# Kernel tuning notes

Measured on AMD Instinct MI355X. Metric: run time of the kernel, lower is better.

Reference implementation:

```python
import jax, jax.numpy as jnp
import numpy as np

EMBED = 1024
HEADS = 16
HDIM = EMBED // HEADS  # k_dim == v_dim == 64
MAXPOS = 256
L = 2 * MAXPOS  # rpe table length = 512
B, S = 1, 2048
EPS = 1e-6


def setup_inputs() -> dict:
    key = jax.random.key(0)
    ks = jax.random.split(key, 16)
    def xavier(k, shape):
        fan_in, fan_out = shape[1], shape[0]
        std = (2.0 / (fan_in + fan_out)) ** 0.5
        return jax.random.normal(k, shape, dtype=jnp.float32) * std
    inp = {
        "query": jax.random.normal(ks[0], (B, S, EMBED), dtype=jnp.float32),
        "key":   jax.random.normal(ks[1], (B, S, EMBED), dtype=jnp.float32),
        "value": jax.random.normal(ks[2], (B, S, EMBED), dtype=jnp.float32),
        "pos":   jax.random.randint(ks[3], (B, S, S), 0, L, dtype=jnp.int32),
        "mask":  jnp.ones((B, S, S), dtype=jnp.float32),
        # projections (stored as [out, in] like torch Linear)
        "Wq": xavier(ks[4], (HEADS * HDIM, EMBED)), "bq": jnp.zeros((HEADS * HDIM,), jnp.float32),
        "Wk": xavier(ks[5], (HEADS * HDIM, EMBED)), "bk": jnp.zeros((HEADS * HDIM,), jnp.float32),
        "Wv": xavier(ks[6], (HEADS * HDIM, EMBED)), "bv": jnp.zeros((HEADS * HDIM,), jnp.float32),
        "rpe": jnp.zeros((L, HEADS, HDIM), jnp.float32) + 0.02 * jax.random.normal(ks[7], (L, HEADS, HDIM), dtype=jnp.float32),
        "Wqt": xavier(ks[8], (EMBED, EMBED)), "bqt": jnp.zeros((EMBED,), jnp.float32),
        "Wo": xavier(ks[9], (EMBED, HEADS * HDIM)), "bo": jnp.zeros((EMBED,), jnp.float32),
        "gamma": jnp.ones((EMBED,), jnp.float32),
        "beta": jnp.zeros((EMBED,), jnp.float32),
    }
    return inp


def _layer_norm(x, gamma, beta):
    mu = jnp.mean(x, axis=-1, keepdims=True)
    var = jnp.mean(jnp.square(x - mu), axis=-1, keepdims=True)
    return (x - mu) * jax.lax.rsqrt(var + EPS) * gamma + beta


def reference(query, key, value, pos, mask, Wq, bq, Wk, bk, Wv, bv, rpe, Wqt, bqt, Wo, bo, gamma, beta):
    b, s, _ = query.shape
    scaling = HDIM ** (-0.5)
    q = (query @ Wq.T + bq) * scaling          # [b,s,n*d]
    k = key @ Wk.T + bk
    v = value @ Wv.T + bv
    q = q.reshape(b, s, HEADS, HDIM)
    k = k.reshape(b, s, HEADS, HDIM)
    v = v.reshape(b, s, HEADS, HDIM)
    attn = jnp.einsum('bqnd,bknd->bqkn', q, k)          # [b,q,k,n]
    qrpe = jnp.einsum('bqnd,lnd->bqln', q, rpe)         # [b,q,L,n]
    idx = jnp.broadcast_to(pos[..., None], (b, s, s, HEADS))
    qrpe_g = jnp.take_along_axis(qrpe, idx, axis=2)     # gather per (q,k) pair
    attn = attn + qrpe_g
    attn = attn - (1.0 - mask[..., None]) * 1e6
    attn = jax.nn.softmax(attn, axis=-2)                # softmax over key axis
    out = jnp.einsum('bqkn,bknd->bqnd', attn, v).reshape(b, s, HEADS * HDIM)
    out = (out @ Wo.T + bo) + (query @ Wqt.T + bqt)
    return _layer_norm(out, gamma, beta)
```

## Files before the change

### kernel.cpp

```cpp
#include <hip/hip_runtime.h>


typedef short          bf16x8 __attribute__((ext_vector_type(8)));
typedef float          f32x4  __attribute__((ext_vector_type(4)));
typedef int            i32x4  __attribute__((ext_vector_type(4)));
typedef unsigned short u16x4  __attribute__((ext_vector_type(4)));
typedef unsigned short u16x8  __attribute__((ext_vector_type(8)));
typedef unsigned int   u32x2  __attribute__((ext_vector_type(2)));

#define SEQ 2048
#define EMB 1024
#define NH  16
#define HD  64
#define RL  512

#define MFMA16(a,b,c) __builtin_amdgcn_mfma_f32_16x16x32_bf16((a),(b),(c),0,0,0)

__device__ __forceinline__ unsigned short f2bf(float f){
  union{float f; unsigned u;} x; x.f=f;
  unsigned r = x.u + 0x7FFFu + ((x.u>>16)&1u);
  return (unsigned short)(r>>16);
}
__device__ __forceinline__ unsigned cvtpk(float a, float b){
  unsigned r;
  asm("v_cvt_pk_bf16_f32 %0, %1, %2" : "=v"(r) : "v"(a), "v"(b));
  return r;
}
__device__ __forceinline__ float fexp2(float x){
  float r; asm("v_exp_f32 %0, %1" : "=v"(r) : "v"(x)); return r;
}
__device__ __forceinline__ unsigned char f2e5(float f){
  union{_Float16 h; unsigned short u;} cv; cv.h = (_Float16)f;
  unsigned short b = cv.u;
  unsigned r = (unsigned)b + 0x7Fu + ((b>>8)&1u);
  return (unsigned char)(r>>8);
}
__device__ __forceinline__ float e52f(unsigned short b){
  union{unsigned short u; _Float16 h;} cv; cv.u = (unsigned short)(b<<8);
  return (float)cv.h;
}
__device__ __forceinline__ void gload16(const void* g, void* l){
  __builtin_amdgcn_global_load_lds((const __attribute__((address_space(1))) unsigned int*)g,
                                   (__attribute__((address_space(3))) unsigned int*)l, 16, 0, 0);
}
__device__ __forceinline__ bf16x8 fragld(const unsigned short* t, int row, int chunk){
  int swz = chunk ^ (row & 7);
  return *(const bf16x8*)(t + row*64 + swz*8);
}

__global__ __launch_bounds__(256) void cvt_all(
    const float* __restrict__ s0, const float* __restrict__ s1, const float* __restrict__ s2,
    const float* __restrict__ s3, const float* __restrict__ s4, const float* __restrict__ s5,
    const float* __restrict__ s6, const float* __restrict__ s7,
    unsigned short* __restrict__ d0, unsigned short* __restrict__ d1, unsigned short* __restrict__ d2,
    unsigned short* __restrict__ d3, unsigned short* __restrict__ d4, unsigned short* __restrict__ d5,
    unsigned short* __restrict__ d6, unsigned short* __restrict__ d7,
    const float* __restrict__ rpe, unsigned short* __restrict__ rpe_bf)
{
  if (blockIdx.y == 8) {
    int i = (blockIdx.x*256 + threadIdx.x)*4;
    if (i >= RL*NH*HD) return;
    int l = i >> 10, h = (i >> 6) & 15, d = i & 63;
    f32x4 a = *(const f32x4*)(rpe + i);
    u16x4 o;
    #pragma unroll
    for (int j=0;j<4;++j) o[j]=f2bf(a[j]);
    *(u16x4*)(rpe_bf + ((size_t)h*RL + l)*HD + d) = o;
    return;
  }
  const float* s; unsigned short* d; int n;
  switch (blockIdx.y) {
    case 0: s=s0; d=d0; n=SEQ*EMB; break;
    case 1: s=s1; d=d1; n=SEQ*EMB; break;
    case 2: s=s2; d=d2; n=SEQ*EMB; break;
    case 3: s=s3; d=d3; n=EMB*EMB; break;
    case 4: s=s4; d=d4; n=EMB*EMB; break;
    case 5: s=s5; d=d5; n=EMB*EMB; break;
    case 6: s=s6; d=d6; n=EMB*EMB; break;
    default: s=s7; d=d7; n=EMB*EMB; break;
  }
  int i = (blockIdx.x*256 + threadIdx.x)*8;
  if (i >= n) return;
  f32x4 a = *(const f32x4*)(s+i);
  f32x4 b = *(const f32x4*)(s+i+4);
  u16x8 o;
  #pragma unroll
  for (int j=0;j<4;++j){ o[j]=f2bf(a[j]); o[4+j]=f2bf(b[j]); }
  *(u16x8*)(d+i) = o;
}

__global__ __launch_bounds__(256) void pack_pm(const int* __restrict__ pos,
                                               const float* __restrict__ mask,
                                               unsigned short* __restrict__ pm)
{
  int i = (blockIdx.x*256 + threadIdx.x)*8;
  i32x4 p0 = *(const i32x4*)(pos + i);
  i32x4 p1 = *(const i32x4*)(pos + i + 4);
  f32x4 m0 = *(const f32x4*)(mask + i);
  f32x4 m1 = *(const f32x4*)(mask + i + 4);
  u16x4 lo, hi;
  #pragma unroll
  for (int j=0;j<4;++j){
    lo[j] = (m0[j] > 0.5f) ? (unsigned short)p0[j] : (unsigned short)512;
    hi[j] = (m1[j] > 0.5f) ? (unsigned short)p1[j] : (unsigned short)512;
  }
  int grp = i & ~31;
  int o0  = ((i & 15) >> 2)*8 + ((i >> 4) & 1)*4;
  *(u16x4*)(pm + grp + o0)     = lo;
  *(u16x4*)(pm + grp + o0 + 8) = hi;
}

__device__ __forceinline__ void gemm_core(const unsigned short* __restrict__ A,
                                          const unsigned short* __restrict__ W,
                                          unsigned short* At, unsigned short* Wt,
                                          f32x4 acc[4][4], int m0, int n0)
{
  const int tid = threadIdx.x, lane = tid & 63, w = tid >> 6;
  const int rg = lane >> 3, sc = (lane & 7) ^ rg;
  const int c = lane & 15, g = lane >> 4;
  const int wm = w >> 1, wn = w & 1;

  for (int kt = 0; kt < EMB/64; ++kt) {
    __syncthreads();
    #pragma unroll
    for (int i = 0; i < 4; ++i) {
      int r = w*32 + i*8 + rg;
      gload16(A + (size_t)(m0+r)*EMB + kt*64 + sc*8, At + (w*32 + i*8)*64);
      gload16(W + (size_t)(n0+r)*EMB + kt*64 + sc*8, Wt + (w*32 + i*8)*64);
    }
    __syncthreads();
    #pragma unroll
    for (int kk = 0; kk < 2; ++kk) {
      bf16x8 af[4], bw[4];
      #pragma unroll
      for (int mf = 0; mf < 4; ++mf) af[mf] = fragld(At, wm*64 + mf*16 + c, kk*4 + g);
      #pragma unroll
      for (int nf = 0; nf < 4; ++nf) bw[nf] = fragld(Wt, wn*64 + nf*16 + c, kk*4 + g);
      __builtin_amdgcn_s_setprio(1);
      #pragma unroll
      for (int mf = 0; mf < 4; ++mf)
        #pragma unroll
        for (int nf = 0; nf < 4; ++nf)
          acc[mf][nf] = MFMA16(af[mf], bw[nf], acc[mf][nf]);
      __builtin_amdgcn_s_setprio(0);
    }
  }
}

__global__ __launch_bounds__(256) void gemm_proj(
    const unsigned short* __restrict__ Aq, const unsigned short* __restrict__ Ak,
    const unsigned short* __restrict__ Av,
    const unsigned short* __restrict__ Wq, const unsigned short* __restrict__ Wk,
    const unsigned short* __restrict__ Wv, const unsigned short* __restrict__ Wqt,
    const float* __restrict__ bq, const float* __restrict__ bk,
    const float* __restrict__ bv, const float* __restrict__ bqt,
    unsigned short* __restrict__ q_out, unsigned short* __restrict__ k_out,
    unsigned short* __restrict__ vt_out, float* __restrict__ qt_out)
{
  __shared__ alignas(16) unsigned short At[128*64];
  __shared__ alignas(16) unsigned short Wt[128*64];
  const unsigned short *A, *W; const float* bias;
  const int z = blockIdx.z;
  if      (z == 0) { A=Aq; W=Wq;  bias=bq;  }
  else if (z == 1) { A=Ak; W=Wk;  bias=bk;  }
  else if (z == 2) { A=Av; W=Wv;  bias=bv;  }
  else             { A=Aq; W=Wqt; bias=bqt; }

  f32x4 acc[4][4];
  #pragma unroll
  for (int i=0;i<4;++i)
    #pragma unroll
    for (int j=0;j<4;++j) acc[i][j] = (f32x4){0.f,0.f,0.f,0.f};

  const int m0 = blockIdx.y*128, n0 = blockIdx.x*128;
  gemm_core(A, W, At, Wt, acc, m0, n0);

  const int lane = threadIdx.x & 63, w = threadIdx.x >> 6;
  const int c = lane & 15, g = lane >> 4, wm = w >> 1, wn = w & 1;
  const float QSCALE = 0.125f * 1.4426950408889634f;
  #pragma unroll
  for (int nf = 0; nf < 4; ++nf) {
    int n = n0 + wn*64 + nf*16 + c;
    float b = bias[n];
    #pragma unroll
    for (int mf = 0; mf < 4; ++mf) {
      int mb = m0 + wm*64 + mf*16 + g*4;
      if (z == 0) {
        #pragma unroll
        for (int j=0;j<4;++j) q_out[(size_t)(mb+j)*EMB + n] = f2bf((acc[mf][nf][j] + b)*QSCALE);
      } else if (z == 1) {
        #pragma unroll
        for (int j=0;j<4;++j) k_out[(size_t)(mb+j)*EMB + n] = f2bf(acc[mf][nf][j] + b);
      } else if (z == 2) {
        u16x4 pk;
        #pragma unroll
        for (int j=0;j<4;++j) pk[j] = f2bf(acc[mf][nf][j] + b);
        *(u16x4*)(vt_out + (size_t)n*SEQ + mb) = pk;
      } else {
        #pragma unroll
        for (int j=0;j<4;++j) qt_out[(size_t)(mb+j)*EMB + n] = acc[mf][nf][j] + b;
      }
    }
  }
}

__global__ __launch_bounds__(256) void gemm_wo(
    const unsigned short* __restrict__ A, const unsigned short* __restrict__ W,
    const float* __restrict__ bo, float* __restrict__ qt)
{
  __shared__ alignas(16) unsigned short At[128*64];
  __shared__ alignas(16) unsigned short Wt[128*64];
  f32x4 acc[4][4];
  #pragma unroll
  for (int i=0;i<4;++i)
    #pragma unroll
    for (int j=0;j<4;++j) acc[i][j] = (f32x4){0.f,0.f,0.f,0.f};
  const int m0 = blockIdx.y*128, n0 = blockIdx.x*128;
  gemm_core(A, W, At, Wt, acc, m0, n0);

  const int lane = threadIdx.x & 63, w = threadIdx.x >> 6;
  const int c = lane & 15, g = lane >> 4, wm = w >> 1, wn = w & 1;
  #pragma unroll
  for (int nf = 0; nf < 4; ++nf) {
    int n = n0 + wn*64 + nf*16 + c;
    float b = bo[n];
    #pragma unroll
    for (int mf = 0; mf < 4; ++mf) {
      int mb = m0 + wm*64 + mf*16 + g*4;
      #pragma unroll
      for (int j=0;j<4;++j) {
        size_t idx = (size_t)(mb+j)*EMB + n;
        qt[idx] = acc[mf][nf][j] + b + qt[idx];
      }
    }
  }
}

__global__ __launch_bounds__(256) void attn_kernel(
    const unsigned short* __restrict__ q_bf, const unsigned short* __restrict__ k_bf,
    const unsigned short* __restrict__ vt_bf, const unsigned short* __restrict__ rpe_bf,
    const unsigned short* __restrict__ pm, unsigned short* __restrict__ att_out)
{
  __shared__ alignas(16) unsigned char pool[38144];
  unsigned short* k_tile  = (unsigned short*)(pool);
  unsigned short* vt_tile = (unsigned short*)(pool + 8192);
  unsigned char*  table8  = pool + 16384;
  unsigned short* q_tile  = (unsigned short*)(pool + 33024);
  unsigned short* p_base  = (unsigned short*)(pool + 33024);
  float*          red     = (float*)(pool);
  float*          red2    = (float*)(pool + 8192);

  const int tid = threadIdx.x, lane = tid & 63, w = tid >> 6;
  const int qh = w & 1, ks = w >> 1;
  const int h = blockIdx.y;
  const int q0 = blockIdx.x * 32;
  const int rg = lane >> 3, sc = (lane & 7) ^ rg;
  const int c = lane & 15, g = lane >> 4;
  const bf16x8 kOnes = {16256,16256,16256,16256,16256,16256,16256,16256};

  gload16(q_bf + (size_t)(q0 + w*8 + rg)*EMB + h*HD + sc*8, q_tile + (w*8)*64);
  __syncthreads();

  for (int ch = 0; ch < 8; ++ch) {
    __syncthreads();
    #pragma unroll
    for (int i = 0; i < 2; ++i)
      gload16(rpe_bf + ((size_t)h*RL + ch*64 + w*16 + i*8 + rg)*HD + sc*8,
              k_tile + (w*16 + i*8)*64);
    __syncthreads();
    #pragma unroll
    for (int qq = 0; qq < 2; ++qq) {
      f32x4 dd = (f32x4){0.f,0.f,0.f,0.f};
      dd = MFMA16(fragld(k_tile, w*16 + c, g),     fragld(q_tile, qq*16 + c, g),     dd);
      dd = MFMA16(fragld(k_tile, w*16 + c, 4 + g), fragld(q_tile, qq*16 + c, 4 + g), dd);
      unsigned pk = (unsigned)f2e5(dd[0]) | ((unsigned)f2e5(dd[1])<<8)
                  | ((unsigned)f2e5(dd[2])<<16) | ((unsigned)f2e5(dd[3])<<24);
      *(unsigned*)(table8 + (qq*16 + c)*520 + ch*64 + w*16 + g*4) = pk;
    }
  }
  if (tid < 32) table8[tid*520 + 512] = 0xFC;

  f32x4 oacc[4];
  #pragma unroll
  for (int i=0;i<4;++i) oacc[i] = (f32x4){0.f,0.f,0.f,0.f};
  f32x4 osum = (f32x4){0.f,0.f,0.f,0.f};
  const bf16x8 qf0 = fragld(q_tile, qh*16 + c, g);
  const bf16x8 qf1 = fragld(q_tile, qh*16 + c, 4 + g);
  unsigned short* pw = p_base + w*640;
  const unsigned char* trow = table8 + (qh*16 + c)*520;
  const unsigned short* pmrow = pm + (size_t)(q0 + qh*16 + c)*SEQ + ks*32 + g*8;

  u16x8 pvv = *(const u16x8*)(pmrow);

  for (int kt = 0; kt < SEQ/64; ++kt) {
    const int kb = kt*64;
    __syncthreads();
    #pragma unroll
    for (int i = 0; i < 2; ++i) {
      gload16(k_bf  + (size_t)(kb + w*16 + i*8 + rg)*EMB + h*HD + sc*8, k_tile  + (w*16 + i*8)*64);
      gload16(vt_bf + ((size_t)h*HD + w*16 + i*8 + rg)*SEQ + kb + sc*8, vt_tile + (w*16 + i*8)*64);
    }
    u16x8 pvv_n = *(const u16x8*)(pmrow + ((kb + 64) & (SEQ-1)));
    __syncthreads();

    #pragma unroll
    for (int kf = 0; kf < 2; ++kf) {
      f32x4 sf = (f32x4){0.f,0.f,0.f,0.f};
      __builtin_amdgcn_s_setprio(1);
      sf = MFMA16(fragld(k_tile, ks*32 + kf*16 + c, g),     qf0, sf);
      sf = MFMA16(fragld(k_tile, ks*32 + kf*16 + c, 4 + g), qf1, sf);
      __builtin_amdgcn_s_setprio(0);
      float p0 = fexp2(sf[0] + e52f(trow[pvv[kf*4+0]]));
      float p1 = fexp2(sf[1] + e52f(trow[pvv[kf*4+1]]));
      float p2 = fexp2(sf[2] + e52f(trow[pvv[kf*4+2]]));
      float p3 = fexp2(sf[3] + e52f(trow[pvv[kf*4+3]]));
      u32x2 pk; pk[0] = cvtpk(p0, p1); pk[1] = cvtpk(p2, p3);
      *(u32x2*)(pw + c*40 + kf*16 + g*4) = pk;
    }
    pvv = pvv_n;
    asm volatile("s_waitcnt lgkmcnt(0)" ::: "memory");
    bf16x8 pa = *(const bf16x8*)(pw + c*40 + g*8);
    __builtin_amdgcn_s_setprio(1);
    #pragma unroll
    for (int df = 0; df < 4; ++df)
      oacc[df] = MFMA16(pa, fragld(vt_tile, df*16 + c, ks*4 + g), oacc[df]);
    osum = MFMA16(pa, kOnes, osum);
    __builtin_amdgcn_s_setprio(0);
  }

  __syncthreads();
  if (ks) {
    #pragma unroll
    for (int df = 0; df < 4; ++df)
      *(f32x4*)(&red[(qh*64 + lane)*16 + df*4]) = oacc[df];
    if (c == 0) *(f32x4*)(&red2[(qh*4 + g)*4]) = osum;
  }
  __syncthreads();
  if (!ks) {
    osum += *(const f32x4*)(&red2[(qh*4 + g)*4]);
    #pragma unroll
    for (int df = 0; df < 4; ++df)
      oacc[df] += *(const f32x4*)(&red[(qh*64 + lane)*16 + df*4]);
    #pragma unroll
    for (int j = 0; j < 4; ++j) {
      float inv = 1.0f / osum[j];
      int qrow = q0 + qh*16 + g*4 + j;
      #pragma unroll
      for (int df = 0; df < 4; ++df)
        att_out[(size_t)qrow*EMB + h*HD + df*16 + c] = f2bf(oacc[df][j] * inv);
    }
  }
}

__global__ __launch_bounds__(256) void ln_kernel(const float* __restrict__ x,
                                                 const float* __restrict__ gamma,
                                                 const float* __restrict__ beta,
                                                 float* __restrict__ out)
{
  const int row = blockIdx.x, t = threadIdx.x;
  f32x4 v = *(const f32x4*)(x + (size_t)row*EMB + t*4);
  float s = v[0]+v[1]+v[2]+v[3];
  #pragma unroll
  for (int o = 32; o > 0; o >>= 1) s += __shfl_xor(s, o);
  __shared__ float r1[4], r2[4];
  if ((t & 63) == 0) r1[t >> 6] = s;
  __syncthreads();
  float mean = (r1[0]+r1[1]+r1[2]+r1[3]) * (1.0f/EMB);
  f32x4 d; float q = 0.f;
  #pragma unroll
  for (int j=0;j<4;++j){ d[j] = v[j] - mean; q += d[j]*d[j]; }
  #pragma unroll
  for (int o = 32; o > 0; o >>= 1) q += __shfl_xor(q, o);
  if ((t & 63) == 0) r2[t >> 6] = q;
  __syncthreads();
  float var = (r2[0]+r2[1]+r2[2]+r2[3]) * (1.0f/EMB);
  float rs = rsqrtf(var + 1e-6f);
  f32x4 gg = *(const f32x4*)(gamma + t*4);
  f32x4 bb = *(const f32x4*)(beta  + t*4);
  f32x4 o4;
  #pragma unroll
  for (int j=0;j<4;++j) o4[j] = d[j]*rs*gg[j] + bb[j];
  *(f32x4*)(out + (size_t)row*EMB + t*4) = o4;
}

extern "C" void kernel_launch(void* const* d_in, const int* in_sizes, int n_in,
                              void* d_out, int out_size, void* d_ws, size_t ws_size,
                              hipStream_t stream)
{
  (void)in_sizes; (void)n_in; (void)out_size;
  const float* query = (const float*)d_in[0];
  const float* key   = (const float*)d_in[1];
  const float* value = (const float*)d_in[2];
  const int*   pos   = (const int*)  d_in[3];
  const float* mask  = (const float*)d_in[4];
  const float* Wq    = (const float*)d_in[5];
  const float* bq    = (const float*)d_in[6];
  const float* Wk    = (const float*)d_in[7];
  const float* bk    = (const float*)d_in[8];
  const float* Wv    = (const float*)d_in[9];
  const float* bv    = (const float*)d_in[10];
  const float* rpe   = (const float*)d_in[11];
  const float* Wqt   = (const float*)d_in[12];
  const float* bqt   = (const float*)d_in[13];
  const float* Wo    = (const float*)d_in[14];
  const float* bo    = (const float*)d_in[15];
  const float* gamma = (const float*)d_in[16];
  const float* beta  = (const float*)d_in[17];
  float* out = (float*)d_out;

  char* ws = (char*)d_ws;
  const size_t OFF_QBF   = 0;
  const size_t OFF_KBF   = 4194304;
  const size_t OFF_VTBF  = 8388608;
  const size_t OFF_QRYBF = 12582912;
  const size_t OFF_KEYBF = 16777216;
  const size_t OFF_VALBF = 20971520;
  const size_t OFF_WQ    = 25165824;
  const size_t OFF_WK    = 27262976;
  const size_t OFF_WV    = 29360128;
  const size_t OFF_WQT   = 31457280;
  const size_t OFF_WO    = 33554432;
  const size_t OFF_RPE   = 35651584;
  const size_t OFF_QT    = 36700160;
  const size_t OFF_ATT   = 45088768;
  const size_t WS_NEED   = 49283072;
  if (ws_size < WS_NEED) return;

  unsigned short* q_bf   = (unsigned short*)(ws + OFF_QBF);
  unsigned short* k_bf   = (unsigned short*)(ws + OFF_KBF);
  unsigned short* vt_bf  = (unsigned short*)(ws + OFF_VTBF);
  unsigned short* qry_bf = (unsigned short*)(ws + OFF_QRYBF);
  unsigned short* key_bf = (unsigned short*)(ws + OFF_KEYBF);
  unsigned short* val_bf = (unsigned short*)(ws + OFF_VALBF);
  unsigned short* wq_bf  = (unsigned short*)(ws + OFF_WQ);
  unsigned short* wk_bf  = (unsigned short*)(ws + OFF_WK);
  unsigned short* wv_bf  = (unsigned short*)(ws + OFF_WV);
  unsigned short* wqt_bf = (unsigned short*)(ws + OFF_WQT);
  unsigned short* wo_bf  = (unsigned short*)(ws + OFF_WO);
  unsigned short* rpe_bf = (unsigned short*)(ws + OFF_RPE);
  float*          qt     = (float*)         (ws + OFF_QT);
  unsigned short* att_bf = (unsigned short*)(ws + OFF_ATT);
  unsigned short* pm16   = (unsigned short*)(ws + OFF_QRYBF);

  cvt_all<<<dim3(1024, 9), 256, 0, stream>>>(
      query, key, value, Wq, Wk, Wv, Wqt, Wo,
      qry_bf, key_bf, val_bf, wq_bf, wk_bf, wv_bf, wqt_bf, wo_bf,
      rpe, rpe_bf);
  gemm_proj<<<dim3(8, 16, 4), 256, 0, stream>>>(
      qry_bf, key_bf, val_bf, wq_bf, wk_bf, wv_bf, wqt_bf,
      bq, bk, bv, bqt, q_bf, k_bf, vt_bf, qt);
  pack_pm<<<SEQ*SEQ/2048, 256, 0, stream>>>(pos, mask, pm16);
  attn_kernel<<<dim3(SEQ/32, NH), 256, 0, stream>>>(
      q_bf, k_bf, vt_bf, rpe_bf, pm16, att_bf);
  gemm_wo<<<dim3(8, 16), 256, 0, stream>>>(att_bf, wo_bf, bo, qt);
  ln_kernel<<<2048, 256, 0, stream>>>(qt, gamma, beta, out);
}
```

Measured before the change: 128.2 us.

## Load K and V fragments directly from global memory into registers in attention loop

New measurement: 209.0 us. 1.63x slower.

```diff
diff --git a/kernel.cpp b/kernel.cpp
--- a/kernel.cpp
+++ b/kernel.cpp
@@ -241,12 +241,11 @@
     const unsigned short* __restrict__ vt_bf, const unsigned short* __restrict__ rpe_bf,
     const unsigned short* __restrict__ pm, unsigned short* __restrict__ att_out)
 {
-  __shared__ alignas(16) unsigned char pool[38144];
-  unsigned short* k_tile  = (unsigned short*)(pool);
-  unsigned short* vt_tile = (unsigned short*)(pool + 8192);
-  unsigned char*  table8  = pool + 16384;
-  unsigned short* q_tile  = (unsigned short*)(pool + 33024);
-  unsigned short* p_base  = (unsigned short*)(pool + 33024);
+  __shared__ alignas(16) unsigned char pool[29952];
+  unsigned short* sbuf    = (unsigned short*)(pool);
+  unsigned char*  table8  = pool + 8192;
+  unsigned short* q_tile  = (unsigned short*)(pool + 24832);
+  unsigned short* p_base  = (unsigned short*)(pool + 24832);
   float*          red     = (float*)(pool);
   float*          red2    = (float*)(pool + 8192);
 
@@ -266,13 +265,13 @@
     #pragma unroll
     for (int i = 0; i < 2; ++i)
       gload16(rpe_bf + ((size_t)h*RL + ch*64 + w*16 + i*8 + rg)*HD + sc*8,
-              k_tile + (w*16 + i*8)*64);
+              sbuf + (w*16 + i*8)*64);
     __syncthreads();
     #pragma unroll
     for (int qq = 0; qq < 2; ++qq) {
       f32x4 dd = (f32x4){0.f,0.f,0.f,0.f};
-      dd = MFMA16(fragld(k_tile, w*16 + c, g),     fragld(q_tile, qq*16 + c, g),     dd);
-      dd = MFMA16(fragld(k_tile, w*16 + c, 4 + g), fragld(q_tile, qq*16 + c, 4 + g), dd);
+      dd = MFMA16(fragld(sbuf, w*16 + c, g),     fragld(q_tile, qq*16 + c, g),     dd);
+      dd = MFMA16(fragld(sbuf, w*16 + c, 4 + g), fragld(q_tile, qq*16 + c, 4 + g), dd);
       unsigned pk = (unsigned)f2e5(dd[0]) | ((unsigned)f2e5(dd[1])<<8)
                   | ((unsigned)f2e5(dd[2])<<16) | ((unsigned)f2e5(dd[3])<<24);
       *(unsigned*)(table8 + (qq*16 + c)*520 + ch*64 + w*16 + g*4) = pk;
@@ -289,41 +288,62 @@
   unsigned short* pw = p_base + w*640;
   const unsigned char* trow = table8 + (qh*16 + c)*520;
   const unsigned short* pmrow = pm + (size_t)(q0 + qh*16 + c)*SEQ + ks*32 + g*8;
+  const unsigned short* kbase = k_bf  + (size_t)(ks*32 + c)*EMB + h*HD + g*8;
+  const unsigned short* vrow0 = vt_bf + ((size_t)h*HD +  0 + c)*SEQ + ks*32 + g*8;
+  const unsigned short* vrow1 = vt_bf + ((size_t)h*HD + 16 + c)*SEQ + ks*32 + g*8;
+  const unsigned short* vrow2 = vt_bf + ((size_t)h*HD + 32 + c)*SEQ + ks*32 + g*8;
+  const unsigned short* vrow3 = vt_bf + ((size_t)h*HD + 48 + c)*SEQ + ks*32 + g*8;
 
   u16x8 pvv = *(const u16x8*)(pmrow);
 
-  for (int kt = 0; kt < SEQ/64; ++kt) {
-    const int kb = kt*64;
-    __syncthreads();
-    #pragma unroll
-    for (int i = 0; i < 2; ++i) {
-      gload16(k_bf  + (size_t)(kb + w*16 + i*8 + rg)*EMB + h*HD + sc*8, k_tile  + (w*16 + i*8)*64);
-      gload16(vt_bf + ((size_t)h*HD + w*16 + i*8 + rg)*SEQ + kb + sc*8, vt_tile + (w*16 + i*8)*64);
-    }
-    u16x8 pvv_n = *(const u16x8*)(pmrow + ((kb + 64) & (SEQ-1)));
-    __syncthreads();
-
-    #pragma unroll
-    for (int kf = 0; kf < 2; ++kf) {
-      f32x4 sf = (f32x4){0.f,0.f,0.f,0.f};
-      __builtin_amdgcn_s_setprio(1);
-      sf = MFMA16(fragld(k_tile, ks*32 + kf*16 + c, g),     qf0, sf);
-      sf = MFMA16(fragld(k_tile, ks*32 + kf*16 + c, 4 + g), qf1, sf);
-      __builtin_amdgcn_s_setprio(0);
-      float p0 = fexp2(sf[0] + e52f(trow[pvv[kf*4+0]]));
-      float p1 = fexp2(sf[1] + e52f(trow[pvv[kf*4+1]]));
-      float p2 = fexp2(sf[2] + e52f(trow[pvv[kf*4+2]]));
-      float p3 = fexp2(sf[3] + e52f(trow[pvv[kf*4+3]]));
+  __syncthreads();
+
+  for (int t = 0; t < 32; ++t) {
+    const size_t kbE = (size_t)t * 64 * EMB;
+    bf16x8 ka00 = *(const bf16x8*)(kbase + kbE);
+    bf16x8 ka01 = *(const bf16x8*)(kbase + kbE + 32);
+    bf16x8 ka10 = *(const bf16x8*)(kbase + kbE + (size_t)16*EMB);
+    bf16x8 ka11 = *(const bf16x8*)(kbase + kbE + (size_t)16*EMB + 32);
+    bf16x8 vf0 = *(const bf16x8*)(vrow0 + t*64);
+    bf16x8 vf1 = *(const bf16x8*)(vrow1 + t*64);
+    bf16x8 vf2 = *(const bf16x8*)(vrow2 + t*64);
+    bf16x8 vf3 = *(const bf16x8*)(vrow3 + t*64);
+    u16x8 pvv_n = *(const u16x8*)(pmrow + ((t*64 + 64) & (SEQ-1)));
+
+    __builtin_amdgcn_s_setprio(1);
+    f32x4 sf0 = (f32x4){0.f,0.f,0.f,0.f};
+    sf0 = MFMA16(ka00, qf0, sf0);
+    sf0 = MFMA16(ka01, qf1, sf0);
+    f32x4 sf1 = (f32x4){0.f,0.f,0.f,0.f};
+    sf1 = MFMA16(ka10, qf0, sf1);
+    sf1 = MFMA16(ka11, qf1, sf1);
+    __builtin_amdgcn_s_setprio(0);
+
+    {
+      float p0 = fexp2(sf0[0] + e52f(trow[pvv[0]]));
+      float p1 = fexp2(sf0[1] + e52f(trow[pvv[1]]));
+      float p2 = fexp2(sf0[2] + e52f(trow[pvv[2]]));
+      float p3 = fexp2(sf0[3] + e52f(trow[pvv[3]]));
       u32x2 pk; pk[0] = cvtpk(p0, p1); pk[1] = cvtpk(p2, p3);
-      *(u32x2*)(pw + c*40 + kf*16 + g*4) = pk;
+      *(u32x2*)(pw + c*40 + g*4) = pk;
+    }
+    {
+      float p0 = fexp2(sf1[0] + e52f(trow[pvv[4]]));
+      float p1 = fexp2(sf1[1] + e52f(trow[pvv[5]]));
+      float p2 = fexp2(sf1[2] + e52f(trow[pvv[6]]));
+      float p3 = fexp2(sf1[3] + e52f(trow[pvv[7]]));
+      u32x2 pk; pk[0] = cvtpk(p0, p1); pk[1] = cvtpk(p2, p3);
+      *(u32x2*)(pw + c*40 + 16 + g*4) = pk;
     }
     pvv = pvv_n;
     asm volatile("s_waitcnt lgkmcnt(0)" ::: "memory");
+    __builtin_amdgcn_sched_barrier(0);
     bf16x8 pa = *(const bf16x8*)(pw + c*40 + g*8);
     __builtin_amdgcn_s_setprio(1);
-    #pragma unroll
-    for (int df = 0; df < 4; ++df)
-      oacc[df] = MFMA16(pa, fragld(vt_tile, df*16 + c, ks*4 + g), oacc[df]);
+    oacc[0] = MFMA16(pa, vf0, oacc[0]);
+    oacc[1] = MFMA16(pa, vf1, oacc[1]);
+    oacc[2] = MFMA16(pa, vf2, oacc[2]);
+    oacc[3] = MFMA16(pa, vf3, oacc[3]);
     osum = MFMA16(pa, kOnes, osum);
     __builtin_amdgcn_s_setprio(0);
   }
```

## Register-prefetch next K/V tile during compute instead of direct global-to-LDS loads

Applied to the files above, without the earlier changes.

New measurement: 126.8 us. About the same (-1.1%).

```diff
diff --git a/kernel.cpp b/kernel.cpp
--- a/kernel.cpp
+++ b/kernel.cpp
@@ -290,18 +290,33 @@
   const unsigned char* trow = table8 + (qh*16 + c)*520;
   const unsigned short* pmrow = pm + (size_t)(q0 + qh*16 + c)*SEQ + ks*32 + g*8;
 
+  const unsigned short* kg0 = k_bf  + (size_t)(w*16 +     rg)*EMB + h*HD + sc*8;
+  const unsigned short* kg1 = k_bf  + (size_t)(w*16 + 8 + rg)*EMB + h*HD + sc*8;
+  const unsigned short* vg0 = vt_bf + ((size_t)h*HD + w*16 +     rg)*SEQ + sc*8;
+  const unsigned short* vg1 = vt_bf + ((size_t)h*HD + w*16 + 8 + rg)*SEQ + sc*8;
+  unsigned short* kd0 = k_tile  + (w*16    )*64 + lane*8;
+  unsigned short* kd1 = k_tile  + (w*16 + 8)*64 + lane*8;
+  unsigned short* vd0 = vt_tile + (w*16    )*64 + lane*8;
+  unsigned short* vd1 = vt_tile + (w*16 + 8)*64 + lane*8;
+
   u16x8 pvv = *(const u16x8*)(pmrow);
 
+  bf16x8 kr0 = *(const bf16x8*)(kg0);
+  bf16x8 kr1 = *(const bf16x8*)(kg1);
+  bf16x8 vr0 = *(const bf16x8*)(vg0);
+  bf16x8 vr1 = *(const bf16x8*)(vg1);
+  __syncthreads();
+  *(bf16x8*)kd0 = kr0; *(bf16x8*)kd1 = kr1;
+  *(bf16x8*)vd0 = vr0; *(bf16x8*)vd1 = vr1;
+  __syncthreads();
+
   for (int kt = 0; kt < SEQ/64; ++kt) {
-    const int kb = kt*64;
-    __syncthreads();
-    #pragma unroll
-    for (int i = 0; i < 2; ++i) {
-      gload16(k_bf  + (size_t)(kb + w*16 + i*8 + rg)*EMB + h*HD + sc*8, k_tile  + (w*16 + i*8)*64);
-      gload16(vt_bf + ((size_t)h*HD + w*16 + i*8 + rg)*SEQ + kb + sc*8, vt_tile + (w*16 + i*8)*64);
-    }
-    u16x8 pvv_n = *(const u16x8*)(pmrow + ((kb + 64) & (SEQ-1)));
-    __syncthreads();
+    const int kb2 = ((kt + 1) & 31) * 64;
+    kr0 = *(const bf16x8*)(kg0 + (size_t)kb2*EMB);
+    kr1 = *(const bf16x8*)(kg1 + (size_t)kb2*EMB);
+    vr0 = *(const bf16x8*)(vg0 + kb2);
+    vr1 = *(const bf16x8*)(vg1 + kb2);
+    u16x8 pvv_n = *(const u16x8*)(pmrow + kb2);
 
     #pragma unroll
     for (int kf = 0; kf < 2; ++kf) {
@@ -319,16 +334,22 @@
     }
     pvv = pvv_n;
     asm volatile("s_waitcnt lgkmcnt(0)" ::: "memory");
+    __builtin_amdgcn_sched_barrier(0);
     bf16x8 pa = *(const bf16x8*)(pw + c*40 + g*8);
     __builtin_amdgcn_s_setprio(1);
-    #pragma unroll
-    for (int df = 0; df < 4; ++df)
-      oacc[df] = MFMA16(pa, fragld(vt_tile, df*16 + c, ks*4 + g), oacc[df]);
+    oacc[0] = MFMA16(pa, fragld(vt_tile,  0 + c, ks*4 + g), oacc[0]);
+    oacc[1] = MFMA16(pa, fragld(vt_tile, 16 + c, ks*4 + g), oacc[1]);
+    oacc[2] = MFMA16(pa, fragld(vt_tile, 32 + c, ks*4 + g), oacc[2]);
+    oacc[3] = MFMA16(pa, fragld(vt_tile, 48 + c, ks*4 + g), oacc[3]);
     osum = MFMA16(pa, kOnes, osum);
     __builtin_amdgcn_s_setprio(0);
-  }
-
-  __syncthreads();
+
+    __syncthreads();
+    *(bf16x8*)kd0 = kr0; *(bf16x8*)kd1 = kr1;
+    *(bf16x8*)vd0 = vr0; *(bf16x8*)vd1 = vr1;
+    __syncthreads();
+  }
+
   if (ks) {
     #pragma unroll
     for (int df = 0; df < 4; ++df)
```
